# Performance work log

Hardware: AMD Instinct MI355X
Metric: run time of the kernel (lower is better)

## Reference

```python
import jax, jax.numpy as jnp
import numpy as np
from math import sqrt

NUM_ENT = 100000
NUM_REL = 237  # base; rel table has 2*NUM_REL rows
DIM = 200
HALF = DIM // 2


def _lrelu(x, slope):
    return jnp.where(x >= 0, x, slope * x)


def setup_inputs() -> dict:
    key = jax.random.key(0)
    ks = jax.random.split(key, 20)
    s = 0.02
    inp = {
        'edge_index': jax.random.randint(ks[0], (2, 500000), 0, NUM_ENT),
        'edge_type': jax.random.randint(ks[1], (500000,), 0, 2 * NUM_REL),
        'toTest': jax.random.randint(ks[2], (131072, 2), 0, NUM_ENT),
        'ent_emb': s * jax.random.normal(ks[3], (NUM_ENT, DIM), jnp.float32),
        'rel_emb': s * jax.random.normal(ks[4], (2 * NUM_REL, DIM), jnp.float32),
        'W': s * jax.random.normal(ks[5], (DIM, DIM), jnp.float32),
        'W_loop': s * jax.random.normal(ks[6], (DIM, DIM), jnp.float32),
        'W_rel': s * jax.random.normal(ks[7], (DIM, DIM), jnp.float32),
        'trans_w': s * jax.random.normal(ks[8], (DIM, HALF), jnp.float32),
        'trans_b': jnp.zeros((HALF,), jnp.float32),
        'q_w': s * jax.random.normal(ks[9], (HALF, 128), jnp.float32),
        'q_b': jnp.zeros((128,), jnp.float32),
        'k_w': s * jax.random.normal(ks[10], (HALF, 128), jnp.float32),
        'k_b': jnp.zeros((128,), jnp.float32),
        'w1': s * jax.random.normal(ks[11], (DIM * 2 + 1 + 2 * NUM_REL, 2048), jnp.float32),
        'b1': jnp.zeros((2048,), jnp.float32),
        'w2': s * jax.random.normal(ks[12], (2048, 512), jnp.float32),
        'b2': jnp.zeros((512,), jnp.float32),
        'w3': s * jax.random.normal(ks[13], (512, 1), jnp.float32),
        'b3': jnp.zeros((1,), jnp.float32),
    }
    return inp


def reference(ent_emb, rel_emb, W, W_loop, W_rel, trans_w, trans_b,
              q_w, q_b, k_w, k_b, w1, b1, w2, b2, w3, b3,
              edge_index, edge_type, toTest):
    # --- CompGCN base layer ('sub' composition, degree-normalized scatter-add) ---
    src, dst = edge_index[0], edge_index[1]
    msg = (ent_emb[src] - rel_emb[edge_type]) @ W          # [E, D] gather + GEMM
    deg = jax.ops.segment_sum(jnp.ones_like(dst, jnp.float32), dst, num_segments=NUM_ENT)
    norm = jax.lax.rsqrt(jnp.maximum(deg, 1.0))
    agg = jax.ops.segment_sum(msg, dst, num_segments=NUM_ENT) * norm[:, None]
    all_ent = jnp.tanh(agg + ent_emb @ W_loop)             # [num_ent, D]
    all_rel = rel_emb @ W_rel                              # [2*num_rel, D]

    # --- PairRE test scoring path ---
    head_rel = all_rel[:, :HALF]                           # [2R, D/2]
    tail_rel = all_rel[:, HALF:]
    te = all_ent[toTest]                                   # [N, 2, D] gather
    ee = te @ trans_w + trans_b                            # [N, 2, D/2]
    h_e, t_e = ee[:, 0], ee[:, 1]
    atta = ((h_e @ q_w + q_b) * (t_e @ k_w + k_b)).sum(-1, keepdims=True) / sqrt(DIM)
    relSim = h_e @ head_rel.T - t_e @ tail_rel.T           # [N, 2R]
    cat = jnp.concatenate([te[:, 0], te[:, 1], atta, relSim], axis=1)
    h1 = _lrelu(cat @ w1 + b1, 1e-4)
    h2 = _lrelu(h1 @ w2 + b2, 1e-3)
    return jax.nn.sigmoid(h2 @ w3 + b3)                    # [N, 1]
```

## Files before the change

### kernel.cpp

```cpp
#include <hip/hip_runtime.h>

typedef unsigned short u16;
typedef unsigned long long u64;
typedef __attribute__((ext_vector_type(8))) short bf8;
typedef __attribute__((ext_vector_type(4))) float fx4;

#define N_ENT   100000
#define N_EDGE  500000
#define N_TEST  131072
#define EDIM    200
#define AE_LD   224
#define NB_SCAN 391

__device__ __forceinline__ u16 f2bf(float f) {
  union { float f; unsigned u; } c; c.f = f;
  return (u16)((c.u + 0x7FFFu + ((c.u >> 16) & 1u)) >> 16);
}
__device__ __forceinline__ float bf2f(u16 h) {
  union { unsigned u; float f; } c; c.u = ((unsigned)h) << 16;
  return c.f;
}
__device__ __forceinline__ void gload16(const u16* g, u16* l) {
  __builtin_amdgcn_global_load_lds(
      (const __attribute__((address_space(1))) void*)g,
      (__attribute__((address_space(3))) void*)l, 16, 0, 0);
}

#define BK 32
#define EPS 72

template<int TM, int WN>
__global__ __launch_bounds__(64 * 2 * WN) void gemm_t(
    const u16* __restrict__ A, long lda,
    const u16* __restrict__ B, long ldb,
    u16* __restrict__ out, long ldOut,
    int K, int NBN,
    const int* __restrict__ rowIdx, int idxMode, int mClamp,
    int mValid, int nValid, int nStore,
    const float* __restrict__ bias, int act, float slope,
    const u16* __restrict__ qbuf, const float* __restrict__ auxF,
    float* __restrict__ dotOut)
{
  constexpr int BM = TM * 32;
  constexpr int BN = WN * 64;
  constexpr int WAVES = 2 * WN;
  __shared__ __align__(16) u16 smem[WAVES * 32 * EPS];
  u16* As = smem;
  u16* Bs = smem + BM * BK;
  const int tid  = threadIdx.x;
  const int wave = tid >> 6, lane = tid & 63;
  const int wr = (wave / WN) * (TM * 16), wc = (wave % WN) * 64;
  const int fr = lane & 15, fq = lane >> 4;

  const int nwg = gridDim.x;
  const int orig = blockIdx.x;
  const int q = nwg >> 3, rr = nwg & 7;
  const int xcd = orig & 7, j = orig >> 3;
  const int wgid = (xcd < rr ? xcd * (q + 1) : rr * (q + 1) + (xcd - rr) * q) + j;
  const long bm = (long)(wgid / NBN) * BM;
  const long bn = (long)(wgid % NBN) * BN;

  const int srow = wave * 32;
  const int kc = (((lane & 3) ^ ((lane >> 3) & 3)) * 8);
  long a0[2], a1[2], boff[2];
  #pragma unroll
  for (int h = 0; h < 2; ++h) {
    long gmRow = bm + srow + h * 16 + (lane >> 2);
    long b0, b1;
    if (idxMode == 0) {
      long gm = (gmRow >= mClamp) ? (mClamp - 1) : gmRow;
      b0 = gm * lda; b1 = b0;
    } else if (idxMode == 2) {
      b0 = (long)rowIdx[2 * gmRow] * lda; b1 = b0;
    } else if (idxMode == 3) {
      b0 = (long)rowIdx[2 * gmRow + 1] * lda; b1 = b0;
    } else {
      b0 = (long)rowIdx[2 * gmRow] * lda;
      b1 = (long)rowIdx[2 * gmRow + 1] * lda - 224;
    }
    a0[h] = b0 + kc; a1[h] = b1 + kc;
    boff[h] = (bn + srow + h * 16 + (lane >> 2)) * ldb + kc;
  }

  fx4 zero4 = {0.f, 0.f, 0.f, 0.f};
  fx4 acc[TM][4];
  #pragma unroll
  for (int i = 0; i < TM; ++i)
    #pragma unroll
    for (int j2 = 0; j2 < 4; ++j2) acc[i][j2] = zero4;

  for (int k0 = 0; k0 < K; k0 += BK) {
    __syncthreads();
    const bool lo = (k0 + kc) < 224;
    #pragma unroll
    for (int h = 0; h < 2; ++h) {
      const long ao = (idxMode == 4) ? (lo ? a0[h] : a1[h]) : a0[h];
      gload16(A + ao + k0, &As[(srow + h * 16) * BK]);
      gload16(B + boff[h] + k0, &Bs[(srow + h * 16) * BK]);
    }
    __syncthreads();
    bf8 aF[TM], bF[4];
    const int rslot = (fq ^ ((fr >> 1) & 3)) * 8;
    #pragma unroll
    for (int mt = 0; mt < TM; ++mt)
      aF[mt] = *(const bf8*)&As[(wr + mt * 16 + fr) * BK + rslot];
    #pragma unroll
    for (int nt = 0; nt < 4; ++nt)
      bF[nt] = *(const bf8*)&Bs[(wc + nt * 16 + fr) * BK + rslot];
    #pragma unroll
    for (int mt = 0; mt < TM; ++mt)
      #pragma unroll
      for (int nt = 0; nt < 4; ++nt)
        acc[mt][nt] = __builtin_amdgcn_mfma_f32_16x16x32_bf16(aF[mt], bF[nt], acc[mt][nt], 0, 0, 0);
  }

  if (act == 3 || act == 4) {
    #pragma unroll
    for (int mt = 0; mt < TM; ++mt) {
      #pragma unroll
      for (int r = 0; r < 4; ++r) {
        const long gm = bm + wr + mt * 16 + fq * 4 + r;
        float p = 0.f;
        #pragma unroll
        for (int nt = 0; nt < 4; ++nt) {
          const long gn = bn + wc + nt * 16 + fr;
          float v = acc[mt][nt][r] + bias[gn];
          if (act == 3) p += v * bf2f(qbuf[gm * 128 + gn]);
          else { v = (v >= 0.f) ? v : v * slope; p += v * auxF[gn]; }
        }
        p += __shfl_xor(p, 1, 64); p += __shfl_xor(p, 2, 64);
        p += __shfl_xor(p, 4, 64); p += __shfl_xor(p, 8, 64);
        if (fr == 0 && gm < mValid)
          atomicAdd(&dotOut[gm], (act == 3) ? p * 0.07071067811865475f : p);
      }
    }
    return;
  }

  __syncthreads();
  u16* ep = smem + wave * (32 * EPS);
  #pragma unroll
  for (int p = 0; p < TM / 2; ++p) {
    #pragma unroll
    for (int mt2 = 0; mt2 < 2; ++mt2) {
      const int mt = 2 * p + mt2;
      #pragma unroll
      for (int r = 0; r < 4; ++r) {
        const int lrl = mt2 * 16 + fq * 4 + r;
        const long gm = bm + wr + mt * 16 + fq * 4 + r;
        const float attaV = (act == 5) ? dotOut[gm] : 0.f;
        #pragma unroll
        for (int nt = 0; nt < 4; ++nt) {
          const long gn = bn + wc + nt * 16 + fr;
          float v = 0.f;
          if (gn < nValid) {
            v = acc[mt][nt][r];
            if (bias) v += bias[gn];
            if (act == 1) v = tanhf(v);
            else if (act == 5) { v += attaV * auxF[gn]; v = (v >= 0.f) ? v : v * slope; }
          }
          ep[lrl * EPS + nt * 16 + fr] = f2bf(v);
        }
      }
    }
    #pragma unroll
    for (int it = 0; it < 4; ++it) {
      const int lr = it * 8 + (lane >> 3);
      const int lc = (lane & 7) * 8;
      const long gm = bm + wr + p * 32 + lr;
      const long gn = bn + wc + lc;
      if (gm < mValid && gn + 7 < nStore)
        *(bf8*)(out + gm * ldOut + gn) = *(const bf8*)&ep[lr * EPS + lc];
    }
  }
}

__global__ void hist_kernel(const int* __restrict__ ei, int* __restrict__ cnt) {
  int e = blockIdx.x * 256 + threadIdx.x;
  if (e < N_EDGE) atomicAdd(&cnt[ei[N_EDGE + e]], 1);
}
__global__ void scanA_kernel(const int* __restrict__ cnt, int* __restrict__ offs,
                             int* __restrict__ blockSums) {
  __shared__ int s[256];
  int gid = blockIdx.x * 256 + threadIdx.x;
  int v = (gid < N_ENT) ? cnt[gid] : 0;
  s[threadIdx.x] = v;
  __syncthreads();
  for (int off = 1; off < 256; off <<= 1) {
    int t = (threadIdx.x >= off) ? s[threadIdx.x - off] : 0;
    __syncthreads();
    s[threadIdx.x] += t;
    __syncthreads();
  }
  if (gid < N_ENT) offs[gid] = s[threadIdx.x] - v;
  if (threadIdx.x == 255) blockSums[blockIdx.x] = s[255];
}
__global__ void scanB_kernel(const int* __restrict__ blockSums, int* __restrict__ blockOffs) {
  __shared__ int s[512];
  int v = (threadIdx.x < NB_SCAN) ? blockSums[threadIdx.x] : 0;
  s[threadIdx.x] = v;
  __syncthreads();
  for (int off = 1; off < 512; off <<= 1) {
    int t = (threadIdx.x >= off) ? s[threadIdx.x - off] : 0;
    __syncthreads();
    s[threadIdx.x] += t;
    __syncthreads();
  }
  if (threadIdx.x < NB_SCAN) blockOffs[threadIdx.x] = s[threadIdx.x] - v;
}
__global__ void scanC_kernel(int* __restrict__ offs, const int* __restrict__ blockOffs) {
  int gid = blockIdx.x * 256 + threadIdx.x;
  if (gid < N_ENT) offs[gid] += blockOffs[blockIdx.x];
}
__global__ void place_kernel(const int* __restrict__ ei, const int* __restrict__ et,
                             const int* __restrict__ offs, int* __restrict__ cursor,
                             int* __restrict__ sortedSrc, int* __restrict__ sortedT) {
  int e = blockIdx.x * 256 + threadIdx.x;
  if (e >= N_EDGE) return;
  int dst = ei[N_EDGE + e];
  int pos = offs[dst] + atomicAdd(&cursor[dst], 1);
  sortedSrc[pos] = ei[e];
  sortedT[pos]   = et[e];
}
__global__ void agg_A1_kernel(const int* __restrict__ offs, const int* __restrict__ cnt,
                              const int* __restrict__ sortedSrc, const int* __restrict__ sortedT,
                              const float* __restrict__ ent_emb, const float* __restrict__ rel_emb,
                              u16* __restrict__ A1) {
  const int r = blockIdx.x * 4 + (threadIdx.x >> 6);
  if (r >= N_ENT) return;
  const int lane = threadIdx.x & 63;
  const int beg = offs[r], n = cnt[r];
  u16* row = A1 + (size_t)r * 416;
  if (lane < 50) {
    float4 a = {0.f, 0.f, 0.f, 0.f};
    for (int e = 0; e < n; ++e) {
      const int s = sortedSrc[beg + e], t = sortedT[beg + e];
      float4 x = ((const float4*)(ent_emb + (size_t)s * EDIM))[lane];
      float4 y = ((const float4*)(rel_emb + (size_t)t * EDIM))[lane];
      a.x += x.x - y.x; a.y += x.y - y.y; a.z += x.z - y.z; a.w += x.w - y.w;
    }
    const float nm = rsqrtf(fmaxf((float)n, 1.f));
    u64 p = (u64)f2bf(a.x * nm) | ((u64)f2bf(a.y * nm) << 16)
          | ((u64)f2bf(a.z * nm) << 32) | ((u64)f2bf(a.w * nm) << 48);
    *(u64*)(row + 4 * lane) = p;
    float4 e = ((const float4*)(ent_emb + (size_t)r * EDIM))[lane];
    u64 q = (u64)f2bf(e.x) | ((u64)f2bf(e.y) << 16)
          | ((u64)f2bf(e.z) << 32) | ((u64)f2bf(e.w) << 48);
    *(u64*)(row + 200 + 4 * lane) = q;
  }
  if (lane < 16) row[400 + lane] = 0;
}

__global__ void build_B1T(const float* __restrict__ W, const float* __restrict__ W_loop,
                          u16* __restrict__ B1T)
{
  int idx = blockIdx.x * 256 + threadIdx.x;
  if (idx >= 256 * 416) return;
  int n = idx / 416, k = idx % 416;
  float v = 0.f;
  if (n < 200) {
    if (k < 200) v = W[k * 200 + n];
    else if (k < 400) v = W_loop[(k - 200) * 200 + n];
  }
  B1T[idx] = f2bf(v);
}
__global__ void all_rel_kernel(const float* __restrict__ rel_emb, const float* __restrict__ W_rel,
                               float* __restrict__ all_rel)
{
  int r = blockIdx.x, c = threadIdx.x;
  if (c >= 200) return;
  const float* re = rel_emb + r * 200;
  float a = 0.f;
  for (int k = 0; k < 200; ++k) a += re[k] * W_rel[k * 200 + c];
  all_rel[r * 200 + c] = a;
}
__global__ void pq_kernel(const float* __restrict__ all_rel, const float* __restrict__ w1,
                          float* __restrict__ PQ) {
  int idx = blockIdx.x * 256 + threadIdx.x;
  if (idx >= 2 * 100 * 2048) return;
  int n = idx & 2047, m = (idx >> 11) % 100, sel = idx / 204800;
  float a = 0.f;
  for (int r = 0; r < 474; ++r)
    a += all_rel[r * 200 + sel * 100 + m] * w1[(size_t)(401 + r) * 2048 + n];
  PQ[idx] = a;
}
__global__ void p2_kernel(const float* __restrict__ trans_w, const float* __restrict__ PQ,
                          float* __restrict__ P2) {
  int idx = blockIdx.x * 256 + threadIdx.x;
  if (idx >= 2 * 200 * 2048) return;
  int n = idx & 2047, k = (idx >> 11) % 200, sel = idx / 409600;
  const float* pq = PQ + sel * 204800;
  float a = 0.f;
  for (int m = 0; m < 100; ++m) a += trans_w[k * 100 + m] * pq[m * 2048 + n];
  P2[idx] = a;
}
__global__ void w1eff_kernel(const float* __restrict__ w1, const float* __restrict__ P2,
                             u16* __restrict__ W1eff) {
  int idx = blockIdx.x * 256 + threadIdx.x;
  if (idx >= 2048 * 448) return;
  int n = idx / 448, k = idx % 448;
  float v = 0.f;
  if (k < 200) v = w1[(size_t)k * 2048 + n] + P2[(size_t)k * 2048 + n];
  else if (k >= 224 && k < 424) {
    int kk = k - 224;
    v = w1[(size_t)(200 + kk) * 2048 + n] - P2[409600 + (size_t)kk * 2048 + n];
  }
  W1eff[idx] = f2bf(v);
}
__global__ void b1eff_kernel(const float* __restrict__ b1, const float* __restrict__ trans_b,
                             const float* __restrict__ PQ, float* __restrict__ b1eff) {
  int n = blockIdx.x * 256 + threadIdx.x;
  if (n >= 2048) return;
  float a = b1[n];
  for (int m = 0; m < 100; ++m)
    a += trans_b[m] * (PQ[m * 2048 + n] - PQ[204800 + m * 2048 + n]);
  b1eff[n] = a;
}
__global__ void qkw2_kernel(const float* __restrict__ trans_w, const float* __restrict__ q_w,
                            const float* __restrict__ k_w, u16* __restrict__ qw2T,
                            u16* __restrict__ kw2T) {
  int idx = blockIdx.x * 256 + threadIdx.x;
  if (idx >= 128 * 224) return;
  int j = idx / 224, k = idx % 224;
  float a = 0.f, b = 0.f;
  if (k < 200)
    for (int m = 0; m < 100; ++m) {
      float t = trans_w[k * 100 + m];
      a += t * q_w[m * 128 + j];
      b += t * k_w[m * 128 + j];
    }
  qw2T[idx] = f2bf(a);
  kw2T[idx] = f2bf(b);
}
__global__ void qkb2_kernel(const float* __restrict__ q_b, const float* __restrict__ k_b,
                            const float* __restrict__ trans_b, const float* __restrict__ q_w,
                            const float* __restrict__ k_w, float* __restrict__ qb2,
                            float* __restrict__ kb2) {
  int j = threadIdx.x;
  if (j >= 128) return;
  float a = q_b[j], b = k_b[j];
  for (int m = 0; m < 100; ++m) {
    a += trans_b[m] * q_w[m * 128 + j];
    b += trans_b[m] * k_w[m * 128 + j];
  }
  qb2[j] = a; kb2[j] = b;
}
__global__ void build_w2T(const float* __restrict__ w2, u16* __restrict__ w2T)
{
  long idx = (long)blockIdx.x * 256 + threadIdx.x;
  if (idx >= (long)512 * 2048) return;
  int n = (int)(idx / 2048), k = (int)(idx % 2048);
  w2T[idx] = f2bf(w2[(size_t)k * 512 + n]);
}
__global__ void sigmoid_kernel(const float* __restrict__ logit, const float* __restrict__ b3,
                               float* __restrict__ out) {
  int i = blockIdx.x * 256 + threadIdx.x;
  if (i >= N_TEST) return;
  out[i] = 1.f / (1.f + __expf(-(logit[i] + b3[0])));
}

extern "C" void kernel_launch(void* const* d_in, const int* in_sizes, int n_in,
                              void* d_out, int out_size, void* d_ws, size_t ws_size,
                              hipStream_t stream)
{
  (void)in_sizes; (void)n_in; (void)out_size;
  const int*   edge_index = (const int*)d_in[0];
  const int*   edge_type  = (const int*)d_in[1];
  const int*   toTest     = (const int*)d_in[2];
  const float* ent_emb    = (const float*)d_in[3];
  const float* rel_emb    = (const float*)d_in[4];
  const float* W          = (const float*)d_in[5];
  const float* W_loop     = (const float*)d_in[6];
  const float* W_rel      = (const float*)d_in[7];
  const float* trans_w    = (const float*)d_in[8];
  const float* trans_b    = (const float*)d_in[9];
  const float* q_w        = (const float*)d_in[10];
  const float* q_b        = (const float*)d_in[11];
  const float* k_w        = (const float*)d_in[12];
  const float* k_b        = (const float*)d_in[13];
  const float* w1         = (const float*)d_in[14];
  const float* b1         = (const float*)d_in[15];
  const float* w2         = (const float*)d_in[16];
  const float* b2         = (const float*)d_in[17];
  const float* w3         = (const float*)d_in[18];
  const float* b3         = (const float*)d_in[19];
  float* out = (float*)d_out;

  unsigned char* ws = (unsigned char*)d_ws;
  float* atta    = (float*)(ws + 0);
  float* logit   = (float*)(ws + 524288);
  float* allrel  = (float*)(ws + 1048576);
  u16*   B1T     = (u16*)  (ws + 1427968);
  u16*   W1eff   = (u16*)  (ws + 1640960);
  u16*   qw2T    = (u16*)  (ws + 3475968);
  u16*   kw2T    = (u16*)  (ws + 3533312);
  float* b1eff   = (float*)(ws + 3590656);
  float* qb2     = (float*)(ws + 3598848);
  float* kb2     = (float*)(ws + 3599872);
  u16*   w2T     = (u16*)  (ws + 3600896);
  const size_t X_base = 5698048;
  u16*   all_ent = (u16*)  (ws + X_base);
  u16*   Qbuf    = (u16*)  (ws + X_base + 44800000);
  const size_t Y_base = 84052480;
  u16*   A1      = (u16*)  (ws + Y_base);
  const size_t Z_base = 167252480;

  int*   cnt       = (int*)  (ws + Z_base);
  int*   offs      = (int*)  (ws + Z_base + 400000);
  int*   cursor    = (int*)  (ws + Z_base + 800000);
  int*   blockSums = (int*)  (ws + Z_base + 1200000);
  int*   blockOffs = (int*)  (ws + Z_base + 1202048);
  int*   sortedSrc = (int*)  (ws + Z_base + 1204096);
  int*   sortedT   = (int*)  (ws + Z_base + 3204096);
  float* PQ        = (float*)(ws + Z_base + 5204096);
  float* P2        = (float*)(ws + Z_base + 6842496);

  int CH;
  if      (Z_base + (size_t)131072 * 4096 <= ws_size) CH = 131072;
  else if (Z_base + (size_t)65536  * 4096 <= ws_size) CH = 65536;
  else if (Z_base + (size_t)32768  * 4096 <= ws_size) CH = 32768;
  else if (Z_base + (size_t)16384  * 4096 <= ws_size) CH = 16384;
  else if (Z_base + (size_t)8192   * 4096 <= ws_size) CH = 8192;
  else return;
  u16* h1 = (u16*)(ws + Z_base);
  const int NC = N_TEST / CH;

  hipMemsetAsync(cnt, 0, 400000, stream);
  hipMemsetAsync(cursor, 0, 400000, stream);
  hipMemsetAsync(atta, 0, 524288, stream);
  hipMemsetAsync(logit, 0, 524288, stream);

  hist_kernel<<<(N_EDGE + 255) / 256, 256, 0, stream>>>(edge_index, cnt);
  scanA_kernel<<<NB_SCAN, 256, 0, stream>>>(cnt, offs, blockSums);
  scanB_kernel<<<1, 512, 0, stream>>>(blockSums, blockOffs);
  scanC_kernel<<<NB_SCAN, 256, 0, stream>>>(offs, blockOffs);
  place_kernel<<<(N_EDGE + 255) / 256, 256, 0, stream>>>(edge_index, edge_type, offs, cursor,
                                                         sortedSrc, sortedT);
  agg_A1_kernel<<<(N_ENT + 3) / 4, 256, 0, stream>>>(offs, cnt, sortedSrc, sortedT,
                                                     ent_emb, rel_emb, A1);
  build_B1T<<<(256 * 416) / 256, 256, 0, stream>>>(W, W_loop, B1T);

  gemm_t<4, 2><<<782 * 2, 256, 0, stream>>>(A1, 416, B1T, 416, all_ent, AE_LD,
      416, 2, nullptr, 0, N_ENT, N_ENT, 200, AE_LD, nullptr, 1, 0.f,
      nullptr, nullptr, nullptr);

  all_rel_kernel<<<474, 256, 0, stream>>>(rel_emb, W_rel, allrel);
  pq_kernel<<<(2 * 100 * 2048) / 256, 256, 0, stream>>>(allrel, w1, PQ);
  p2_kernel<<<(2 * 200 * 2048) / 256, 256, 0, stream>>>(trans_w, PQ, P2);
  w1eff_kernel<<<(2048 * 448) / 256, 256, 0, stream>>>(w1, P2, W1eff);
  b1eff_kernel<<<8, 256, 0, stream>>>(b1, trans_b, PQ, b1eff);
  qkw2_kernel<<<(128 * 224) / 256, 256, 0, stream>>>(trans_w, q_w, k_w, qw2T, kw2T);
  qkb2_kernel<<<1, 128, 0, stream>>>(q_b, k_b, trans_b, q_w, k_w, qb2, kb2);
  build_w2T<<<(512 * 2048) / 256, 256, 0, stream>>>(w2, w2T);

  gemm_t<4, 2><<<1024, 256, 0, stream>>>(all_ent, AE_LD, qw2T, AE_LD, Qbuf, 128,
      AE_LD, 1, toTest, 2, 0, N_TEST, 128, 128, qb2, 0, 0.f,
      nullptr, nullptr, nullptr);
  gemm_t<4, 2><<<1024, 256, 0, stream>>>(all_ent, AE_LD, kw2T, AE_LD, nullptr, 0,
      AE_LD, 1, toTest, 3, 0, N_TEST, 128, 128, kb2, 3, 0.f,
      Qbuf, nullptr, atta);

  for (int c = 0; c < NC; ++c) {
    gemm_t<4, 2><<<(CH / 128) * 16, 256, 0, stream>>>(all_ent, AE_LD, W1eff, 448, h1, 2048,
        448, 16, toTest + (size_t)c * CH * 2, 4, 0, CH, 2048, 2048, b1eff, 5, 0.0001f,
        nullptr, w1 + (size_t)400 * 2048, atta + (size_t)c * CH);
    gemm_t<4, 2><<<(CH / 128) * 4, 256, 0, stream>>>(h1, 2048, w2T, 2048, nullptr, 0,
        2048, 4, nullptr, 0, CH, CH, 512, 512, b2, 4, 0.001f,
        nullptr, w3, logit + (size_t)c * CH);
  }
  sigmoid_kernel<<<N_TEST / 256, 256, 0, stream>>>(logit, b3, out);
}
```

Baseline: 1.788 ms.

## Double-buffer LDS tiles in GEMM to overlap global loads with MFMA

```diff
diff --git a/kernel.cpp b/kernel.cpp
--- a/kernel.cpp
+++ b/kernel.cpp
@@ -43,10 +43,8 @@
 {
   constexpr int BM = TM * 32;
   constexpr int BN = WN * 64;
-  constexpr int WAVES = 2 * WN;
-  __shared__ __align__(16) u16 smem[WAVES * 32 * EPS];
-  u16* As = smem;
-  u16* Bs = smem + BM * BK;
+  constexpr int BUFS = (BM + BN) * BK;
+  __shared__ __align__(16) u16 smem[2 * BUFS];
   const int tid  = threadIdx.x;
   const int wave = tid >> 6, lane = tid & 63;
   const int wr = (wave / WN) * (TM * 16), wc = (wave % WN) * 64;
@@ -82,6 +80,18 @@
     boff[h] = (bn + srow + h * 16 + (lane >> 2)) * ldb + kc;
   }
 
+  auto STAGE = [&](int buf, int k0) {
+    u16* Ad = smem + buf * BUFS;
+    u16* Bd = Ad + BM * BK;
+    const bool lo = (k0 + kc) < 224;
+    #pragma unroll
+    for (int h = 0; h < 2; ++h) {
+      const long ao = (idxMode == 4) ? (lo ? a0[h] : a1[h]) : a0[h];
+      gload16(A + ao + k0, &Ad[(srow + h * 16) * BK]);
+      gload16(B + boff[h] + k0, &Bd[(srow + h * 16) * BK]);
+    }
+  };
+
   fx4 zero4 = {0.f, 0.f, 0.f, 0.f};
   fx4 acc[TM][4];
   #pragma unroll
@@ -89,29 +99,41 @@
     #pragma unroll
     for (int j2 = 0; j2 < 4; ++j2) acc[i][j2] = zero4;
 
-  for (int k0 = 0; k0 < K; k0 += BK) {
-    __syncthreads();
-    const bool lo = (k0 + kc) < 224;
-    #pragma unroll
-    for (int h = 0; h < 2; ++h) {
-      const long ao = (idxMode == 4) ? (lo ? a0[h] : a1[h]) : a0[h];
-      gload16(A + ao + k0, &As[(srow + h * 16) * BK]);
-      gload16(B + boff[h] + k0, &Bs[(srow + h * 16) * BK]);
-    }
-    __syncthreads();
-    bf8 aF[TM], bF[4];
-    const int rslot = (fq ^ ((fr >> 1) & 3)) * 8;
-    #pragma unroll
-    for (int mt = 0; mt < TM; ++mt)
-      aF[mt] = *(const bf8*)&As[(wr + mt * 16 + fr) * BK + rslot];
-    #pragma unroll
-    for (int nt = 0; nt < 4; ++nt)
-      bF[nt] = *(const bf8*)&Bs[(wc + nt * 16 + fr) * BK + rslot];
-    #pragma unroll
-    for (int mt = 0; mt < TM; ++mt)
+  const int NT = K / BK;
+  STAGE(0, 0);
+  for (int t = 0; t < NT; ++t) {
+    const int cur = t & 1;
+    if (t + 1 < NT) {
+      STAGE(cur ^ 1, (t + 1) * BK);
+      __builtin_amdgcn_sched_barrier(0);
+      asm volatile("s_waitcnt vmcnt(4)" ::: "memory");
+    } else {
+      __builtin_amdgcn_sched_barrier(0);
+      asm volatile("s_waitcnt vmcnt(0)" ::: "memory");
+    }
+    __builtin_amdgcn_sched_barrier(0);
+    __builtin_amdgcn_s_barrier();
+    __builtin_amdgcn_sched_barrier(0);
+    {
+      const u16* Ac = smem + cur * BUFS;
+      const u16* Bc = Ac + BM * BK;
+      bf8 aF[TM], bF[4];
+      const int rslot = (fq ^ ((fr >> 1) & 3)) * 8;
+      #pragma unroll
+      for (int mt = 0; mt < TM; ++mt)
+        aF[mt] = *(const bf8*)&Ac[(wr + mt * 16 + fr) * BK + rslot];
       #pragma unroll
       for (int nt = 0; nt < 4; ++nt)
-        acc[mt][nt] = __builtin_amdgcn_mfma_f32_16x16x32_bf16(aF[mt], bF[nt], acc[mt][nt], 0, 0, 0);
+        bF[nt] = *(const bf8*)&Bc[(wc + nt * 16 + fr) * BK + rslot];
+      #pragma unroll
+      for (int mt = 0; mt < TM; ++mt)
+        #pragma unroll
+        for (int nt = 0; nt < 4; ++nt)
+          acc[mt][nt] = __builtin_amdgcn_mfma_f32_16x16x32_bf16(aF[mt], bF[nt], acc[mt][nt], 0, 0, 0);
+    }
+    __builtin_amdgcn_sched_barrier(0);
+    __builtin_amdgcn_s_barrier();
+    __builtin_amdgcn_sched_barrier(0);
   }
 
   if (act == 3 || act == 4) {
@@ -137,7 +159,6 @@
     return;
   }
 
-  __syncthreads();
   u16* ep = smem + wave * (32 * EPS);
   #pragma unroll
   for (int p = 0; p < TM / 2; ++p) {
```

Measured after the change: 1.666 ms. 6.8% less time.
